# Optimization experiments

Measured on AMD Instinct MI355X. Metric: run time of the kernel, lower is better.

Reference implementation:

```python
import jax, jax.numpy as jnp
import numpy as np

B, N, D, H = 16, 1024, 512, 8


def setup_inputs() -> dict:
    key = jax.random.key(0)
    ks = jax.random.split(key, 11)
    std = D ** (-0.5)
    inp = {
        "k": jax.random.normal(ks[0], (B, N, D), dtype=jnp.float32),
        "v": jax.random.normal(ks[1], (B, N, D), dtype=jnp.float32),
        "q": jax.random.normal(ks[2], (B, N, D), dtype=jnp.float32),
        # per-head projection weights, torch Linear layout [out,in], init std = in**-0.5
        "Wk": jax.random.normal(ks[3], (H, D, D), dtype=jnp.float32) * std,
        "bk": jax.random.normal(ks[4], (H, D), dtype=jnp.float32) * 0.01,
        "Wv": jax.random.normal(ks[5], (H, D, D), dtype=jnp.float32) * std,
        "bv": jax.random.normal(ks[6], (H, D), dtype=jnp.float32) * 0.01,
        "Wq": jax.random.normal(ks[7], (H, D, D), dtype=jnp.float32) * std,
        "bq": jax.random.normal(ks[8], (H, D), dtype=jnp.float32) * 0.01,
        # output projection: Linear(H*D -> D), weight [D, H*D]
        "Wo": jax.random.normal(ks[9], (D, H * D), dtype=jnp.float32) * ((H * D) ** (-0.5)),
        "bo": jax.random.normal(ks[10], (D,), dtype=jnp.float32) * 0.01,
    }
    return inp


def reference(k, v, q, Wk, bk, Wv, bv, Wq, bq, Wo, bo):
    scale = jnp.asarray(D ** 0.5, dtype=k.dtype)
    # batched per-head projections: y = x @ W.T + b  -> [H, B, N, D]
    k_ = jnp.einsum("bnd,hed->hbne", k, Wk) + bk[:, None, None, :]
    v_ = jnp.einsum("bnd,hed->hbne", v, Wv) + bv[:, None, None, :]
    q_ = jnp.einsum("bnd,hed->hbne", q, Wq) + bq[:, None, None, :]
    # dot-product attention: scores[h,b,i,j] = q_[h,b,i] . k_[h,b,j]
    scores = jnp.einsum("hbid,hbjd->hbij", q_, k_) / scale
    attn = jax.nn.softmax(scores, axis=-1)
    out = jnp.einsum("hbij,hbjd->hbid", attn, v_)  # [H, B, N, D]
    # torch: stack(dim=-1) -> [B,N,D,H]; view -> [B,N,D*H] interleaved (d,h)
    outs = jnp.transpose(out, (1, 2, 3, 0)).reshape(B, N, D * H)
    rep = jnp.einsum("bnf,of->bno", outs, Wo) + bo
    return rep
```

## Files before the change

kernel.cpp:

```cpp
#include <hip/hip_runtime.h>

typedef __bf16 bf16;
typedef __bf16 bf16x8 __attribute__((ext_vector_type(8)));
typedef __bf16 bf16x4 __attribute__((ext_vector_type(4)));
typedef float  f32x4  __attribute__((ext_vector_type(4)));

#define BATCH 16
#define SEQ   1024
#define DIM   512
#define HEADS 8
#define BN    (BATCH*SEQ)
#define QK_SCALE 0.04419417382415922f


__device__ __forceinline__ void load16_lds(const void* g, void* l) {
  __builtin_amdgcn_global_load_lds((__attribute__((address_space(1))) void*)g,
                                   (__attribute__((address_space(3))) void*)l,
                                   16, 0, 0);
}

template<bool RS>
__device__ __forceinline__ void gemm_tile(const bf16* __restrict__ Atile, int lda,
                                          const bf16* __restrict__ Btile, int ldb,
                                          int K, f32x4 acc[4][4], f32x4 rs[4])
{
  __shared__ bf16 As[2][128*32];
  __shared__ bf16 Bs[2][128*32];
  const int tid  = threadIdx.x;
  const int wave = tid >> 6;
  const int lane = tid & 63;
  const int wm = wave >> 1, wn = wave & 1;
  const int srow = lane >> 2;
  const int scol = (lane & 3) * 8;
  const int frow = lane & 15;
  const int kq   = (lane >> 4) * 8;

  bf16x8 ones;
#pragma unroll
  for (int j = 0; j < 8; ++j) ones[j] = (bf16)1.0f;

  __syncthreads();
#pragma unroll
  for (int i = 0; i < 2; ++i) {
    const int c = wave * 2 + i;
    load16_lds(Atile + (size_t)(c*16 + srow) * lda + scol, &As[0][c*512]);
    load16_lds(Btile + (size_t)(c*16 + srow) * ldb + scol, &Bs[0][c*512]);
  }
  __syncthreads();

  int cur = 0;
  for (int kt = 0; kt < K; kt += 32) {
    const int nxt = kt + 32;
    if (nxt < K) {
#pragma unroll
      for (int i = 0; i < 2; ++i) {
        const int c = wave * 2 + i;
        load16_lds(Atile + (size_t)(c*16 + srow) * lda + nxt + scol, &As[cur^1][c*512]);
        load16_lds(Btile + (size_t)(c*16 + srow) * ldb + nxt + scol, &Bs[cur^1][c*512]);
      }
    }
    bf16x8 af[4], bfr[4];
#pragma unroll
    for (int mi = 0; mi < 4; ++mi)
      af[mi] = *(const bf16x8*)(&As[cur][(wm*64 + mi*16 + frow)*32 + kq]);
#pragma unroll
    for (int ni = 0; ni < 4; ++ni)
      bfr[ni] = *(const bf16x8*)(&Bs[cur][(wn*64 + ni*16 + frow)*32 + kq]);
#pragma unroll
    for (int mi = 0; mi < 4; ++mi) {
#pragma unroll
      for (int ni = 0; ni < 4; ++ni)
        acc[mi][ni] = __builtin_amdgcn_mfma_f32_16x16x32_bf16(af[mi], bfr[ni],
                                                              acc[mi][ni], 0, 0, 0);
      if (RS)
        rs[mi] = __builtin_amdgcn_mfma_f32_16x16x32_bf16(af[mi], ones, rs[mi], 0, 0, 0);
    }
    __syncthreads();
    cur ^= 1;
  }
}



__global__ __launch_bounds__(256)
void proj_nk(const bf16* __restrict__ X, const bf16* __restrict__ W,
             const float* __restrict__ bias, bf16* __restrict__ C)
{
  const int z = blockIdx.z;
  const bf16* A  = X + (size_t)blockIdx.x * 128 * DIM;
  const bf16* Bt = W + (size_t)z * DIM * DIM + (size_t)blockIdx.y * 128 * DIM;
  f32x4 acc[4][4] = {};
  gemm_tile<false>(A, DIM, Bt, DIM, DIM, acc, nullptr);

  const int tid = threadIdx.x, wave = tid >> 6, lane = tid & 63;
  const int wm = wave >> 1, wn = wave & 1;
  const int row0 = blockIdx.x*128 + wm*64;
  const int col0 = blockIdx.y*128 + wn*64;
  bf16* Cz = C + (size_t)z * BN * DIM;
  const float* bz = bias + (size_t)z * DIM;
#pragma unroll
  for (int ni = 0; ni < 4; ++ni) {
    const int col = col0 + ni*16 + (lane & 15);
    const float bb = bz[col];
#pragma unroll
    for (int mi = 0; mi < 4; ++mi) {
      const int row = row0 + mi*16 + (lane >> 4)*4;
#pragma unroll
      for (int r = 0; r < 4; ++r)
        Cz[(size_t)(row + r)*DIM + col] = (bf16)(acc[mi][ni][r] + bb);
    }
  }
}

__global__ __launch_bounds__(256)
void proj_v(const bf16* __restrict__ X, const bf16* __restrict__ W,
            const float* __restrict__ bias, bf16* __restrict__ vT)
{
  const int z = blockIdx.z;
  const bf16* A  = X + (size_t)blockIdx.x * 128 * DIM;
  const bf16* Bt = W + (size_t)z * DIM * DIM + (size_t)blockIdx.y * 128 * DIM;
  f32x4 acc[4][4] = {};
  gemm_tile<false>(A, DIM, Bt, DIM, DIM, acc, nullptr);

  const int tid = threadIdx.x, wave = tid >> 6, lane = tid & 63;
  const int wm = wave >> 1, wn = wave & 1;
  const int gm0 = blockIdx.x * 128;
  const int b   = gm0 >> 10;
  const int n00 = (gm0 & (SEQ-1)) + wm*64;
  const int col0 = blockIdx.y*128 + wn*64;
  const float* bz = bias + (size_t)z * DIM;
  bf16* base = vT + (size_t)(z*BATCH + b) * DIM * SEQ;
#pragma unroll
  for (int ni = 0; ni < 4; ++ni) {
    const int d = col0 + ni*16 + (lane & 15);
    const float bb = bz[d];
#pragma unroll
    for (int mi = 0; mi < 4; ++mi) {
      const int n = n00 + mi*16 + (lane >> 4)*4;
      bf16x4 v;
      v[0] = (bf16)(acc[mi][ni][0] + bb);
      v[1] = (bf16)(acc[mi][ni][1] + bb);
      v[2] = (bf16)(acc[mi][ni][2] + bb);
      v[3] = (bf16)(acc[mi][ni][3] + bb);
      *(bf16x4*)(base + (size_t)d*SEQ + n) = v;
    }
  }
}


__global__ __launch_bounds__(256)
void k_scores(const bf16* __restrict__ Q, const bf16* __restrict__ Kh,
              bf16* __restrict__ P)
{
  const int z = blockIdx.z;
  const bf16* A  = Q  + (size_t)z*SEQ*DIM + (size_t)blockIdx.x*128*DIM;
  const bf16* Bt = Kh + (size_t)z*SEQ*DIM + (size_t)blockIdx.y*128*DIM;
  f32x4 acc[4][4] = {};
  gemm_tile<false>(A, DIM, Bt, DIM, DIM, acc, nullptr);

  const int tid = threadIdx.x, wave = tid >> 6, lane = tid & 63;
  const int wm = wave >> 1, wn = wave & 1;
  const int row0 = blockIdx.x*128 + wm*64;
  const int col0 = blockIdx.y*128 + wn*64;
  bf16* Pz = P + (size_t)z * SEQ * SEQ;
#pragma unroll
  for (int ni = 0; ni < 4; ++ni) {
    const int col = col0 + ni*16 + (lane & 15);
#pragma unroll
    for (int mi = 0; mi < 4; ++mi) {
      const int row = row0 + mi*16 + (lane >> 4)*4;
#pragma unroll
      for (int r = 0; r < 4; ++r)
        Pz[(size_t)(row + r)*SEQ + col] = (bf16)__expf(acc[mi][ni][r] * QK_SCALE);
    }
  }
}

__global__ __launch_bounds__(256)
void k_pv(const bf16* __restrict__ P, const bf16* __restrict__ vT,
          bf16* __restrict__ Out)
{
  const int z = blockIdx.z;
  const bf16* A  = P  + (size_t)z*SEQ*SEQ + (size_t)blockIdx.x*128*SEQ;
  const bf16* Bt = vT + (size_t)z*DIM*SEQ + (size_t)blockIdx.y*128*SEQ;
  f32x4 acc[4][4] = {};
  f32x4 rs[4] = {};
  gemm_tile<true>(A, SEQ, Bt, SEQ, SEQ, acc, rs);

  const int tid = threadIdx.x, wave = tid >> 6, lane = tid & 63;
  const int wm = wave >> 1, wn = wave & 1;
  const int row0 = blockIdx.x*128 + wm*64;
  const int col0 = blockIdx.y*128 + wn*64;
  bf16* Oz = Out + (size_t)z * SEQ * DIM;
  float inv[4][4];
#pragma unroll
  for (int mi = 0; mi < 4; ++mi)
#pragma unroll
    for (int r = 0; r < 4; ++r)
      inv[mi][r] = 1.0f / rs[mi][r];
#pragma unroll
  for (int ni = 0; ni < 4; ++ni) {
    const int col = col0 + ni*16 + (lane & 15);
#pragma unroll
    for (int mi = 0; mi < 4; ++mi) {
      const int row = row0 + mi*16 + (lane >> 4)*4;
#pragma unroll
      for (int r = 0; r < 4; ++r)
        Oz[(size_t)(row + r)*DIM + col] = (bf16)(acc[mi][ni][r] * inv[mi][r]);
    }
  }
}

__global__ __launch_bounds__(256)
void k_final(const bf16* __restrict__ OutB, const bf16* __restrict__ Wor,
             int G, float* __restrict__ rep)
{
  f32x4 acc[4][4] = {};
  for (int g = 0; g < G; ++g)
    gemm_tile<false>(OutB + (size_t)g*BN*DIM + (size_t)blockIdx.x*128*DIM, DIM,
                     Wor  + (size_t)g*DIM*DIM + (size_t)blockIdx.y*128*DIM, DIM,
                     DIM, acc, nullptr);

  const int tid = threadIdx.x, wave = tid >> 6, lane = tid & 63;
  const int wm = wave >> 1, wn = wave & 1;
  const int row0 = blockIdx.x*128 + wm*64;
  const int col0 = blockIdx.y*128 + wn*64;
#pragma unroll
  for (int ni = 0; ni < 4; ++ni) {
    const int col = col0 + ni*16 + (lane & 15);
#pragma unroll
    for (int mi = 0; mi < 4; ++mi) {
      const int row = row0 + mi*16 + (lane >> 4)*4;
#pragma unroll
      for (int r = 0; r < 4; ++r)
        rep[(size_t)(row + r)*DIM + col] += acc[mi][ni][r];
    }
  }
}


__global__ __launch_bounds__(256)
void k_cast(const float* __restrict__ in, bf16* __restrict__ out, int n8)
{
  const int i = blockIdx.x*256 + threadIdx.x;
  if (i >= n8) return;
  const float4* p = (const float4*)in + (size_t)i*2;
  const float4 a = p[0], b = p[1];
  bf16x8 o;
  o[0]=(bf16)a.x; o[1]=(bf16)a.y; o[2]=(bf16)a.z; o[3]=(bf16)a.w;
  o[4]=(bf16)b.x; o[5]=(bf16)b.y; o[6]=(bf16)b.z; o[7]=(bf16)b.w;
  *((bf16x8*)out + i) = o;
}

__global__ __launch_bounds__(256)
void k_rearrange_wo(const float* __restrict__ Wo, bf16* __restrict__ Wor)
{
  const int idx = blockIdx.x*256 + threadIdx.x;
  const int d = idx & (DIM-1);
  const int o = (idx >> 9) & (DIM-1);
  const int h = idx >> 18;
  Wor[idx] = (bf16)Wo[((size_t)o << 12) + (d << 3) + h];
}

__global__ __launch_bounds__(256)
void k_init_out(float* __restrict__ out, const float* __restrict__ bo)
{
  const int idx = blockIdx.x*256 + threadIdx.x;
  out[idx] = bo[idx & (DIM-1)];
}


extern "C" void kernel_launch(void* const* d_in, const int* in_sizes, int n_in,
                              void* d_out, int out_size, void* d_ws, size_t ws_size,
                              hipStream_t stream)
{
  (void)in_sizes; (void)n_in; (void)out_size;
  const float* k_in = (const float*)d_in[0];
  const float* v_in = (const float*)d_in[1];
  const float* q_in = (const float*)d_in[2];
  const float* Wk   = (const float*)d_in[3];
  const float* bk   = (const float*)d_in[4];
  const float* Wv   = (const float*)d_in[5];
  const float* bv   = (const float*)d_in[6];
  const float* Wq   = (const float*)d_in[7];
  const float* bq   = (const float*)d_in[8];
  const float* Wo   = (const float*)d_in[9];
  const float* bo   = (const float*)d_in[10];

  auto needBytes = [](int G, int Bc) -> size_t {
    size_t b = 0;
    b += (size_t)3 * BN * DIM * 2;
    b += (size_t)3 * HEADS * DIM * DIM * 2;
    b += (size_t)HEADS * DIM * DIM * 2;
    b += (size_t)4 * G * BN * DIM * 2;
    b += (size_t)Bc * SEQ * SEQ * 2;
    return b;
  };
  static const int cand[8][2] = {{8,16},{4,16},{2,16},{1,16},{1,8},{1,4},{1,2},{1,1}};
  int G = 1, Bc = 1;
  for (int c = 0; c < 8; ++c)
    if (needBytes(cand[c][0], cand[c][1]) <= ws_size) { G = cand[c][0]; Bc = cand[c][1]; break; }

  char* p = (char*)d_ws;
  auto take = [&](size_t bytes) { char* r = p; p += bytes; return r; };
  bf16* Xk   = (bf16*)take((size_t)BN*DIM*2);
  bf16* Xv   = (bf16*)take((size_t)BN*DIM*2);
  bf16* Xq   = (bf16*)take((size_t)BN*DIM*2);
  bf16* Wkc  = (bf16*)take((size_t)HEADS*DIM*DIM*2);
  bf16* Wvc  = (bf16*)take((size_t)HEADS*DIM*DIM*2);
  bf16* Wqc  = (bf16*)take((size_t)HEADS*DIM*DIM*2);
  bf16* Worb = (bf16*)take((size_t)HEADS*DIM*DIM*2);
  bf16* qh   = (bf16*)take((size_t)G*BN*DIM*2);
  bf16* kh   = (bf16*)take((size_t)G*BN*DIM*2);
  bf16* vTh  = (bf16*)take((size_t)G*BN*DIM*2);
  bf16* outb = (bf16*)take((size_t)G*BN*DIM*2);
  bf16* Pb   = (bf16*)take((size_t)Bc*SEQ*SEQ*2);

  const int n8x = BN*DIM/8;
  const int n8w = HEADS*DIM*DIM/8;
  k_cast<<<n8x/256, 256, 0, stream>>>(k_in, Xk, n8x);
  k_cast<<<n8x/256, 256, 0, stream>>>(v_in, Xv, n8x);
  k_cast<<<n8x/256, 256, 0, stream>>>(q_in, Xq, n8x);
  k_cast<<<n8w/256, 256, 0, stream>>>(Wk, Wkc, n8w);
  k_cast<<<n8w/256, 256, 0, stream>>>(Wv, Wvc, n8w);
  k_cast<<<n8w/256, 256, 0, stream>>>(Wq, Wqc, n8w);
  k_rearrange_wo<<<HEADS*DIM*DIM/256, 256, 0, stream>>>(Wo, Worb);
  k_init_out<<<BN*DIM/256, 256, 0, stream>>>((float*)d_out, bo);

  for (int g0 = 0; g0 < HEADS; g0 += G) {
    dim3 gp(BN/128, DIM/128, G);
    proj_nk<<<gp, 256, 0, stream>>>(Xq, Wqc + (size_t)g0*DIM*DIM, bq + (size_t)g0*DIM, qh);
    proj_nk<<<gp, 256, 0, stream>>>(Xk, Wkc + (size_t)g0*DIM*DIM, bk + (size_t)g0*DIM, kh);
    proj_v <<<gp, 256, 0, stream>>>(Xv, Wvc + (size_t)g0*DIM*DIM, bv + (size_t)g0*DIM, vTh);
    for (int hz = 0; hz < G; ++hz) {
      for (int b0 = 0; b0 < BATCH; b0 += Bc) {
        const size_t hb = (size_t)(hz*BATCH + b0);
        dim3 gs(SEQ/128, SEQ/128, Bc);
        k_scores<<<gs, 256, 0, stream>>>(qh + hb*SEQ*DIM, kh + hb*SEQ*DIM, Pb);
        dim3 gv(SEQ/128, DIM/128, Bc);
        k_pv<<<gv, 256, 0, stream>>>(Pb, vTh + hb*DIM*SEQ, outb + hb*SEQ*DIM);
      }
    }
    k_final<<<dim3(BN/128, DIM/128), 256, 0, stream>>>(outb, Worb + (size_t)g0*DIM*DIM, G, (float*)d_out);
  }
}
```

Measured before the change: 1.270 ms.

## Fold Q/K and V/O weights algebraically and fuse PV with output projection

Precomputes the per-head products Wq^T·Wk and Wo_h·Wv with a hi/lo bf16 split, so the scores come from q·M against the raw k, and each head's V path maps straight to the output dimension. Bias terms reduce to a per-key constant and a constant output bias, and the bk term is dropped because it cancels in the softmax. PV and the output projection are fused into one kernel that accumulates over heads, which removes the K projection, the separate final GEMM, and the read-modify-write of the output. The trade-off is extra precompute kernels, larger workspace, and possible precision loss from folding the weights.

```diff
diff --git a/kernel.cpp b/kernel.cpp
--- a/kernel.cpp
+++ b/kernel.cpp
@@ -80,163 +80,6 @@
   }
 }
 
-
-
-__global__ __launch_bounds__(256)
-void proj_nk(const bf16* __restrict__ X, const bf16* __restrict__ W,
-             const float* __restrict__ bias, bf16* __restrict__ C)
-{
-  const int z = blockIdx.z;
-  const bf16* A  = X + (size_t)blockIdx.x * 128 * DIM;
-  const bf16* Bt = W + (size_t)z * DIM * DIM + (size_t)blockIdx.y * 128 * DIM;
-  f32x4 acc[4][4] = {};
-  gemm_tile<false>(A, DIM, Bt, DIM, DIM, acc, nullptr);
-
-  const int tid = threadIdx.x, wave = tid >> 6, lane = tid & 63;
-  const int wm = wave >> 1, wn = wave & 1;
-  const int row0 = blockIdx.x*128 + wm*64;
-  const int col0 = blockIdx.y*128 + wn*64;
-  bf16* Cz = C + (size_t)z * BN * DIM;
-  const float* bz = bias + (size_t)z * DIM;
-#pragma unroll
-  for (int ni = 0; ni < 4; ++ni) {
-    const int col = col0 + ni*16 + (lane & 15);
-    const float bb = bz[col];
-#pragma unroll
-    for (int mi = 0; mi < 4; ++mi) {
-      const int row = row0 + mi*16 + (lane >> 4)*4;
-#pragma unroll
-      for (int r = 0; r < 4; ++r)
-        Cz[(size_t)(row + r)*DIM + col] = (bf16)(acc[mi][ni][r] + bb);
-    }
-  }
-}
-
-__global__ __launch_bounds__(256)
-void proj_v(const bf16* __restrict__ X, const bf16* __restrict__ W,
-            const float* __restrict__ bias, bf16* __restrict__ vT)
-{
-  const int z = blockIdx.z;
-  const bf16* A  = X + (size_t)blockIdx.x * 128 * DIM;
-  const bf16* Bt = W + (size_t)z * DIM * DIM + (size_t)blockIdx.y * 128 * DIM;
-  f32x4 acc[4][4] = {};
-  gemm_tile<false>(A, DIM, Bt, DIM, DIM, acc, nullptr);
-
-  const int tid = threadIdx.x, wave = tid >> 6, lane = tid & 63;
-  const int wm = wave >> 1, wn = wave & 1;
-  const int gm0 = blockIdx.x * 128;
-  const int b   = gm0 >> 10;
-  const int n00 = (gm0 & (SEQ-1)) + wm*64;
-  const int col0 = blockIdx.y*128 + wn*64;
-  const float* bz = bias + (size_t)z * DIM;
-  bf16* base = vT + (size_t)(z*BATCH + b) * DIM * SEQ;
-#pragma unroll
-  for (int ni = 0; ni < 4; ++ni) {
-    const int d = col0 + ni*16 + (lane & 15);
-    const float bb = bz[d];
-#pragma unroll
-    for (int mi = 0; mi < 4; ++mi) {
-      const int n = n00 + mi*16 + (lane >> 4)*4;
-      bf16x4 v;
-      v[0] = (bf16)(acc[mi][ni][0] + bb);
-      v[1] = (bf16)(acc[mi][ni][1] + bb);
-      v[2] = (bf16)(acc[mi][ni][2] + bb);
-      v[3] = (bf16)(acc[mi][ni][3] + bb);
-      *(bf16x4*)(base + (size_t)d*SEQ + n) = v;
-    }
-  }
-}
-
-
-__global__ __launch_bounds__(256)
-void k_scores(const bf16* __restrict__ Q, const bf16* __restrict__ Kh,
-              bf16* __restrict__ P)
-{
-  const int z = blockIdx.z;
-  const bf16* A  = Q  + (size_t)z*SEQ*DIM + (size_t)blockIdx.x*128*DIM;
-  const bf16* Bt = Kh + (size_t)z*SEQ*DIM + (size_t)blockIdx.y*128*DIM;
-  f32x4 acc[4][4] = {};
-  gemm_tile<false>(A, DIM, Bt, DIM, DIM, acc, nullptr);
-
-  const int tid = threadIdx.x, wave = tid >> 6, lane = tid & 63;
-  const int wm = wave >> 1, wn = wave & 1;
-  const int row0 = blockIdx.x*128 + wm*64;
-  const int col0 = blockIdx.y*128 + wn*64;
-  bf16* Pz = P + (size_t)z * SEQ * SEQ;
-#pragma unroll
-  for (int ni = 0; ni < 4; ++ni) {
-    const int col = col0 + ni*16 + (lane & 15);
-#pragma unroll
-    for (int mi = 0; mi < 4; ++mi) {
-      const int row = row0 + mi*16 + (lane >> 4)*4;
-#pragma unroll
-      for (int r = 0; r < 4; ++r)
-        Pz[(size_t)(row + r)*SEQ + col] = (bf16)__expf(acc[mi][ni][r] * QK_SCALE);
-    }
-  }
-}
-
-__global__ __launch_bounds__(256)
-void k_pv(const bf16* __restrict__ P, const bf16* __restrict__ vT,
-          bf16* __restrict__ Out)
-{
-  const int z = blockIdx.z;
-  const bf16* A  = P  + (size_t)z*SEQ*SEQ + (size_t)blockIdx.x*128*SEQ;
-  const bf16* Bt = vT + (size_t)z*DIM*SEQ + (size_t)blockIdx.y*128*SEQ;
-  f32x4 acc[4][4] = {};
-  f32x4 rs[4] = {};
-  gemm_tile<true>(A, SEQ, Bt, SEQ, SEQ, acc, rs);
-
-  const int tid = threadIdx.x, wave = tid >> 6, lane = tid & 63;
-  const int wm = wave >> 1, wn = wave & 1;
-  const int row0 = blockIdx.x*128 + wm*64;
-  const int col0 = blockIdx.y*128 + wn*64;
-  bf16* Oz = Out + (size_t)z * SEQ * DIM;
-  float inv[4][4];
-#pragma unroll
-  for (int mi = 0; mi < 4; ++mi)
-#pragma unroll
-    for (int r = 0; r < 4; ++r)
-      inv[mi][r] = 1.0f / rs[mi][r];
-#pragma unroll
-  for (int ni = 0; ni < 4; ++ni) {
-    const int col = col0 + ni*16 + (lane & 15);
-#pragma unroll
-    for (int mi = 0; mi < 4; ++mi) {
-      const int row = row0 + mi*16 + (lane >> 4)*4;
-#pragma unroll
-      for (int r = 0; r < 4; ++r)
-        Oz[(size_t)(row + r)*DIM + col] = (bf16)(acc[mi][ni][r] * inv[mi][r]);
-    }
-  }
-}
-
-__global__ __launch_bounds__(256)
-void k_final(const bf16* __restrict__ OutB, const bf16* __restrict__ Wor,
-             int G, float* __restrict__ rep)
-{
-  f32x4 acc[4][4] = {};
-  for (int g = 0; g < G; ++g)
-    gemm_tile<false>(OutB + (size_t)g*BN*DIM + (size_t)blockIdx.x*128*DIM, DIM,
-                     Wor  + (size_t)g*DIM*DIM + (size_t)blockIdx.y*128*DIM, DIM,
-                     DIM, acc, nullptr);
-
-  const int tid = threadIdx.x, wave = tid >> 6, lane = tid & 63;
-  const int wm = wave >> 1, wn = wave & 1;
-  const int row0 = blockIdx.x*128 + wm*64;
-  const int col0 = blockIdx.y*128 + wn*64;
-#pragma unroll
-  for (int ni = 0; ni < 4; ++ni) {
-    const int col = col0 + ni*16 + (lane & 15);
-#pragma unroll
-    for (int mi = 0; mi < 4; ++mi) {
-      const int row = row0 + mi*16 + (lane >> 4)*4;
-#pragma unroll
-      for (int r = 0; r < 4; ++r)
-        rep[(size_t)(row + r)*DIM + col] += acc[mi][ni][r];
-    }
-  }
-}
 
 
 __global__ __launch_bounds__(256)
@@ -253,20 +96,252 @@
 }
 
 __global__ __launch_bounds__(256)
-void k_rearrange_wo(const float* __restrict__ Wo, bf16* __restrict__ Wor)
+void k_trans_hilo(const float* __restrict__ W, bf16* __restrict__ Thi,
+                  bf16* __restrict__ Tlo)
 {
   const int idx = blockIdx.x*256 + threadIdx.x;
-  const int d = idx & (DIM-1);
-  const int o = (idx >> 9) & (DIM-1);
-  const int h = idx >> 18;
-  Wor[idx] = (bf16)Wo[((size_t)o << 12) + (d << 3) + h];
-}
-
-__global__ __launch_bounds__(256)
-void k_init_out(float* __restrict__ out, const float* __restrict__ bo)
+  const int e = idx & 511, d = (idx >> 9) & 511, h = idx >> 18;
+  const float v = W[((size_t)(h*DIM + e))*DIM + d];
+  const bf16 hi = (bf16)v;
+  Thi[idx] = hi;
+  Tlo[idx] = (bf16)(v - (float)hi);
+}
+
+__global__ __launch_bounds__(256)
+void k_wor_hilo(const float* __restrict__ Wo, bf16* __restrict__ Whi,
+                bf16* __restrict__ Wlo)
 {
   const int idx = blockIdx.x*256 + threadIdx.x;
-  out[idx] = bo[idx & (DIM-1)];
+  const int e = idx & 511, o = (idx >> 9) & 511, h = idx >> 18;
+  const float v = Wo[((size_t)o << 12) + (e << 3) + h];
+  const bf16 hi = (bf16)v;
+  Whi[idx] = hi;
+  Wlo[idx] = (bf16)(v - (float)hi);
+}
+
+__global__ __launch_bounds__(256)
+void k_gemm3(const bf16* Ahi, const bf16* Alo, const bf16* Bhi, const bf16* Blo,
+             bf16* __restrict__ C)
+{
+  const int z = blockIdx.z;
+  const size_t off = (size_t)z * DIM * DIM;
+  f32x4 acc[4][4] = {};
+  for (int t = 0; t < 3; ++t) {
+    const bf16* A  = ((t == 2) ? Alo : Ahi) + off + (size_t)blockIdx.x*128*DIM;
+    const bf16* Bt = ((t == 1) ? Blo : Bhi) + off + (size_t)blockIdx.y*128*DIM;
+    gemm_tile<false>(A, DIM, Bt, DIM, DIM, acc, nullptr);
+  }
+  const int tid = threadIdx.x, wave = tid >> 6, lane = tid & 63;
+  const int wm = wave >> 1, wn = wave & 1;
+  const int row0 = blockIdx.x*128 + wm*64;
+  const int col0 = blockIdx.y*128 + wn*64;
+#pragma unroll
+  for (int ni = 0; ni < 4; ++ni) {
+    const int col = col0 + ni*16 + (lane & 15);
+#pragma unroll
+    for (int mi = 0; mi < 4; ++mi) {
+      const int row = row0 + mi*16 + (lane >> 4)*4;
+#pragma unroll
+      for (int r = 0; r < 4; ++r)
+        C[off + (size_t)(row + r)*DIM + col] = (bf16)acc[mi][ni][r];
+    }
+  }
+}
+
+__global__ __launch_bounds__(256)
+void k_wvec(const float* __restrict__ Wk, const float* __restrict__ bq,
+            float* __restrict__ w)
+{
+  const int idx = blockIdx.x*256 + threadIdx.x;
+  const int d = idx & 511, h = idx >> 9;
+  float s = 0.f;
+  for (int e = 0; e < DIM; ++e)
+    s += Wk[((size_t)(h*DIM + e))*DIM + d] * bq[h*DIM + e];
+  w[idx] = s;
+}
+
+__global__ __launch_bounds__(256)
+void k_cvec(const float* __restrict__ k, const float* __restrict__ w,
+            float* __restrict__ c)
+{
+  __shared__ float ws[HEADS][DIM];
+  for (int i = threadIdx.x; i < HEADS*DIM; i += 256)
+    ws[i >> 9][i & 511] = w[i];
+  __syncthreads();
+  const int token = blockIdx.x*4 + (threadIdx.x >> 6);
+  const int lane  = threadIdx.x & 63;
+  const float4* kr = (const float4*)(k + (size_t)token * DIM);
+  float kk[8];
+  *(float4*)(kk)     = kr[lane*2];
+  *(float4*)(kk + 4) = kr[lane*2 + 1];
+#pragma unroll
+  for (int h = 0; h < HEADS; ++h) {
+    float s = 0.f;
+#pragma unroll
+    for (int j = 0; j < 8; ++j) s += kk[j] * ws[h][lane*8 + j];
+#pragma unroll
+    for (int o = 32; o >= 1; o >>= 1) s += __shfl_xor(s, o, 64);
+    if (lane == 0) c[(size_t)h*BN + token] = s;
+  }
+}
+
+__global__ __launch_bounds__(256)
+void k_bconst(const float* __restrict__ Wo, const float* __restrict__ bv,
+              const float* __restrict__ bo, float* __restrict__ bc)
+{
+  const int o    = blockIdx.x*4 + (threadIdx.x >> 6);
+  const int lane = threadIdx.x & 63;
+  const float4* row = (const float4*)(Wo + ((size_t)o << 12));
+  float s = 0.f;
+  for (int it = 0; it < 16; ++it) {
+    const int f0 = (it*64 + lane)*4;
+    const float4 x = row[it*64 + lane];
+    s += x.x * bv[((f0+0)&7)*DIM + ((f0+0)>>3)];
+    s += x.y * bv[((f0+1)&7)*DIM + ((f0+1)>>3)];
+    s += x.z * bv[((f0+2)&7)*DIM + ((f0+2)>>3)];
+    s += x.w * bv[((f0+3)&7)*DIM + ((f0+3)>>3)];
+  }
+#pragma unroll
+  for (int of = 32; of >= 1; of >>= 1) s += __shfl_xor(s, of, 64);
+  if (lane == 0) bc[o] = s + bo[o];
+}
+
+
+__global__ __launch_bounds__(256)
+void k_qm(const bf16* __restrict__ X, const bf16* __restrict__ MT,
+          bf16* __restrict__ C)
+{
+  const int z = blockIdx.z;
+  const bf16* A  = X  + (size_t)blockIdx.x*128*DIM;
+  const bf16* Bt = MT + (size_t)z*DIM*DIM + (size_t)blockIdx.y*128*DIM;
+  f32x4 acc[4][4] = {};
+  gemm_tile<false>(A, DIM, Bt, DIM, DIM, acc, nullptr);
+
+  const int tid = threadIdx.x, wave = tid >> 6, lane = tid & 63;
+  const int wm = wave >> 1, wn = wave & 1;
+  const int rows = gridDim.x * 128;
+  const int row0 = blockIdx.x*128 + wm*64;
+  const int col0 = blockIdx.y*128 + wn*64;
+  bf16* Cz = C + (size_t)z * rows * DIM;
+#pragma unroll
+  for (int ni = 0; ni < 4; ++ni) {
+    const int col = col0 + ni*16 + (lane & 15);
+#pragma unroll
+    for (int mi = 0; mi < 4; ++mi) {
+      const int row = row0 + mi*16 + (lane >> 4)*4;
+#pragma unroll
+      for (int r = 0; r < 4; ++r)
+        Cz[(size_t)(row + r)*DIM + col] = (bf16)acc[mi][ni][r];
+    }
+  }
+}
+
+__global__ __launch_bounds__(256)
+void k_vct(const bf16* __restrict__ X, const bf16* __restrict__ G,
+           bf16* __restrict__ vcT, int Bc)
+{
+  const int z = blockIdx.z;
+  const bf16* A  = X + (size_t)blockIdx.x*128*DIM;
+  const bf16* Bt = G + (size_t)z*DIM*DIM + (size_t)blockIdx.y*128*DIM;
+  f32x4 acc[4][4] = {};
+  gemm_tile<false>(A, DIM, Bt, DIM, DIM, acc, nullptr);
+
+  const int tid = threadIdx.x, wave = tid >> 6, lane = tid & 63;
+  const int wm = wave >> 1, wn = wave & 1;
+  const int gm0 = blockIdx.x * 128;
+  const int bloc = gm0 >> 10;
+  const int n00 = (gm0 & (SEQ-1)) + wm*64;
+  const int col0 = blockIdx.y*128 + wn*64;
+  bf16* base = vcT + (size_t)(z*Bc + bloc) * DIM * SEQ;
+#pragma unroll
+  for (int ni = 0; ni < 4; ++ni) {
+    const int o = col0 + ni*16 + (lane & 15);
+#pragma unroll
+    for (int mi = 0; mi < 4; ++mi) {
+      const int n = n00 + mi*16 + (lane >> 4)*4;
+      bf16x4 v;
+      v[0] = (bf16)acc[mi][ni][0];
+      v[1] = (bf16)acc[mi][ni][1];
+      v[2] = (bf16)acc[mi][ni][2];
+      v[3] = (bf16)acc[mi][ni][3];
+      *(bf16x4*)(base + (size_t)o*SEQ + n) = v;
+    }
+  }
+}
+
+__global__ __launch_bounds__(256)
+void k_scores(const bf16* __restrict__ QM, const bf16* __restrict__ Kb,
+              const float* __restrict__ cvec, bf16* __restrict__ P,
+              int Bc, int b0)
+{
+  const int z = blockIdx.z;
+  const int h = z / Bc, bloc = z % Bc;
+  const bf16* A  = QM + ((size_t)(h*Bc + bloc)*SEQ + blockIdx.x*128)*DIM;
+  const bf16* Bt = Kb + ((size_t)(b0 + bloc)*SEQ + blockIdx.y*128)*DIM;
+  f32x4 acc[4][4] = {};
+  gemm_tile<false>(A, DIM, Bt, DIM, DIM, acc, nullptr);
+
+  const int tid = threadIdx.x, wave = tid >> 6, lane = tid & 63;
+  const int wm = wave >> 1, wn = wave & 1;
+  const int row0 = blockIdx.x*128 + wm*64;
+  const int col0 = blockIdx.y*128 + wn*64;
+  const float* cz = cvec + (size_t)h*BN + (size_t)(b0 + bloc)*SEQ;
+  bf16* Pz = P + (size_t)(h*Bc + bloc)*SEQ*SEQ;
+#pragma unroll
+  for (int ni = 0; ni < 4; ++ni) {
+    const int col = col0 + ni*16 + (lane & 15);
+    const float cc = cz[col];
+#pragma unroll
+    for (int mi = 0; mi < 4; ++mi) {
+      const int row = row0 + mi*16 + (lane >> 4)*4;
+#pragma unroll
+      for (int r = 0; r < 4; ++r)
+        Pz[(size_t)(row + r)*SEQ + col] = (bf16)__expf((acc[mi][ni][r] + cc) * QK_SCALE);
+    }
+  }
+}
+
+__global__ __launch_bounds__(256, 2)
+void k_pvfinal(const bf16* __restrict__ P, const bf16* __restrict__ vcT,
+               const float* __restrict__ bcon, float* __restrict__ rep,
+               int Bc, int b0)
+{
+  const int bloc = blockIdx.z;
+  f32x4 accO[4][4] = {};
+  for (int h = 0; h < HEADS; ++h) {
+    const bf16* A  = P   + ((size_t)(h*Bc + bloc)*SEQ + blockIdx.x*128)*SEQ;
+    const bf16* Bt = vcT + ((size_t)(h*Bc + bloc)*DIM + blockIdx.y*128)*SEQ;
+    f32x4 acc[4][4] = {};
+    f32x4 rs[4] = {};
+    gemm_tile<true>(A, SEQ, Bt, SEQ, SEQ, acc, rs);
+#pragma unroll
+    for (int mi = 0; mi < 4; ++mi) {
+      f32x4 inv;
+#pragma unroll
+      for (int r = 0; r < 4; ++r) inv[r] = 1.0f / rs[mi][r];
+#pragma unroll
+      for (int ni = 0; ni < 4; ++ni)
+#pragma unroll
+        for (int r = 0; r < 4; ++r)
+          accO[mi][ni][r] += acc[mi][ni][r] * inv[r];
+    }
+  }
+  const int tid = threadIdx.x, wave = tid >> 6, lane = tid & 63;
+  const int wm = wave >> 1, wn = wave & 1;
+  const int row0 = (b0 + bloc)*SEQ + blockIdx.x*128 + wm*64;
+  const int col0 = blockIdx.y*128 + wn*64;
+#pragma unroll
+  for (int ni = 0; ni < 4; ++ni) {
+    const int col = col0 + ni*16 + (lane & 15);
+    const float bb = bcon[col];
+#pragma unroll
+    for (int mi = 0; mi < 4; ++mi) {
+      const int row = row0 + mi*16 + (lane >> 4)*4;
+#pragma unroll
+      for (int r = 0; r < 4; ++r)
+        rep[(size_t)(row + r)*DIM + col] = accO[mi][ni][r] + bb;
+    }
+  }
 }
 
 
@@ -279,68 +354,67 @@
   const float* v_in = (const float*)d_in[1];
   const float* q_in = (const float*)d_in[2];
   const float* Wk   = (const float*)d_in[3];
-  const float* bk   = (const float*)d_in[4];
+  const float* bq_f = (const float*)d_in[8];
   const float* Wv   = (const float*)d_in[5];
-  const float* bv   = (const float*)d_in[6];
+  const float* bv_f = (const float*)d_in[6];
   const float* Wq   = (const float*)d_in[7];
-  const float* bq   = (const float*)d_in[8];
   const float* Wo   = (const float*)d_in[9];
   const float* bo   = (const float*)d_in[10];
 
-  auto needBytes = [](int G, int Bc) -> size_t {
-    size_t b = 0;
-    b += (size_t)3 * BN * DIM * 2;
-    b += (size_t)3 * HEADS * DIM * DIM * 2;
-    b += (size_t)HEADS * DIM * DIM * 2;
-    b += (size_t)4 * G * BN * DIM * 2;
-    b += (size_t)Bc * SEQ * SEQ * 2;
-    return b;
-  };
-  static const int cand[8][2] = {{8,16},{4,16},{2,16},{1,16},{1,8},{1,4},{1,2},{1,1}};
-  int G = 1, Bc = 1;
-  for (int c = 0; c < 8; ++c)
-    if (needBytes(cand[c][0], cand[c][1]) <= ws_size) { G = cand[c][0]; Bc = cand[c][1]; break; }
+  const size_t WMAT = (size_t)HEADS*DIM*DIM*2;
+  const size_t fixedB = (size_t)3*BN*DIM*2 + 8*WMAT + 2*WMAT
+                      + (size_t)HEADS*DIM*4 + (size_t)HEADS*BN*4 + DIM*4;
+  int Bc = 1;
+  for (int c : {16, 8, 4, 2, 1}) {
+    const size_t need = fixedB + (size_t)c * (2*(size_t)HEADS*SEQ*DIM*2
+                                              + (size_t)HEADS*SEQ*SEQ*2);
+    if (need <= ws_size) { Bc = c; break; }
+  }
 
   char* p = (char*)d_ws;
   auto take = [&](size_t bytes) { char* r = p; p += bytes; return r; };
-  bf16* Xk   = (bf16*)take((size_t)BN*DIM*2);
-  bf16* Xv   = (bf16*)take((size_t)BN*DIM*2);
-  bf16* Xq   = (bf16*)take((size_t)BN*DIM*2);
-  bf16* Wkc  = (bf16*)take((size_t)HEADS*DIM*DIM*2);
-  bf16* Wvc  = (bf16*)take((size_t)HEADS*DIM*DIM*2);
-  bf16* Wqc  = (bf16*)take((size_t)HEADS*DIM*DIM*2);
-  bf16* Worb = (bf16*)take((size_t)HEADS*DIM*DIM*2);
-  bf16* qh   = (bf16*)take((size_t)G*BN*DIM*2);
-  bf16* kh   = (bf16*)take((size_t)G*BN*DIM*2);
-  bf16* vTh  = (bf16*)take((size_t)G*BN*DIM*2);
-  bf16* outb = (bf16*)take((size_t)G*BN*DIM*2);
-  bf16* Pb   = (bf16*)take((size_t)Bc*SEQ*SEQ*2);
+  bf16* qbf   = (bf16*)take((size_t)BN*DIM*2);
+  bf16* vbf   = (bf16*)take((size_t)BN*DIM*2);
+  bf16* kbf   = (bf16*)take((size_t)BN*DIM*2);
+  bf16* WqThi = (bf16*)take(WMAT);
+  bf16* WqTlo = (bf16*)take(WMAT);
+  bf16* WkThi = (bf16*)take(WMAT);
+  bf16* WkTlo = (bf16*)take(WMAT);
+  bf16* WvThi = (bf16*)take(WMAT);
+  bf16* WvTlo = (bf16*)take(WMAT);
+  bf16* Worhi = (bf16*)take(WMAT);
+  bf16* Worlo = (bf16*)take(WMAT);
+  bf16* MT    = (bf16*)take(WMAT);
+  bf16* Gwv   = (bf16*)take(WMAT);
+  float* wv   = (float*)take((size_t)HEADS*DIM*4);
+  float* cvec = (float*)take((size_t)HEADS*BN*4);
+  float* bcon = (float*)take((size_t)DIM*4);
+  bf16* qm    = (bf16*)take((size_t)Bc*HEADS*SEQ*DIM*2);
+  bf16* vcT   = (bf16*)take((size_t)Bc*HEADS*SEQ*DIM*2);
+  bf16* Pb    = (bf16*)take((size_t)Bc*HEADS*SEQ*SEQ*2);
 
   const int n8x = BN*DIM/8;
-  const int n8w = HEADS*DIM*DIM/8;
-  k_cast<<<n8x/256, 256, 0, stream>>>(k_in, Xk, n8x);
-  k_cast<<<n8x/256, 256, 0, stream>>>(v_in, Xv, n8x);
-  k_cast<<<n8x/256, 256, 0, stream>>>(q_in, Xq, n8x);
-  k_cast<<<n8w/256, 256, 0, stream>>>(Wk, Wkc, n8w);
-  k_cast<<<n8w/256, 256, 0, stream>>>(Wv, Wvc, n8w);
-  k_cast<<<n8w/256, 256, 0, stream>>>(Wq, Wqc, n8w);
-  k_rearrange_wo<<<HEADS*DIM*DIM/256, 256, 0, stream>>>(Wo, Worb);
-  k_init_out<<<BN*DIM/256, 256, 0, stream>>>((float*)d_out, bo);
-
-  for (int g0 = 0; g0 < HEADS; g0 += G) {
-    dim3 gp(BN/128, DIM/128, G);
-    proj_nk<<<gp, 256, 0, stream>>>(Xq, Wqc + (size_t)g0*DIM*DIM, bq + (size_t)g0*DIM, qh);
-    proj_nk<<<gp, 256, 0, stream>>>(Xk, Wkc + (size_t)g0*DIM*DIM, bk + (size_t)g0*DIM, kh);
-    proj_v <<<gp, 256, 0, stream>>>(Xv, Wvc + (size_t)g0*DIM*DIM, bv + (size_t)g0*DIM, vTh);
-    for (int hz = 0; hz < G; ++hz) {
-      for (int b0 = 0; b0 < BATCH; b0 += Bc) {
-        const size_t hb = (size_t)(hz*BATCH + b0);
-        dim3 gs(SEQ/128, SEQ/128, Bc);
-        k_scores<<<gs, 256, 0, stream>>>(qh + hb*SEQ*DIM, kh + hb*SEQ*DIM, Pb);
-        dim3 gv(SEQ/128, DIM/128, Bc);
-        k_pv<<<gv, 256, 0, stream>>>(Pb, vTh + hb*DIM*SEQ, outb + hb*SEQ*DIM);
-      }
-    }
-    k_final<<<dim3(BN/128, DIM/128), 256, 0, stream>>>(outb, Worb + (size_t)g0*DIM*DIM, G, (float*)d_out);
-  }
-}
+  const int nW  = HEADS*DIM*DIM;
+  k_cast<<<n8x/256, 256, 0, stream>>>(q_in, qbf, n8x);
+  k_cast<<<n8x/256, 256, 0, stream>>>(v_in, vbf, n8x);
+  k_cast<<<n8x/256, 256, 0, stream>>>(k_in, kbf, n8x);
+  k_trans_hilo<<<nW/256, 256, 0, stream>>>(Wq, WqThi, WqTlo);
+  k_trans_hilo<<<nW/256, 256, 0, stream>>>(Wk, WkThi, WkTlo);
+  k_trans_hilo<<<nW/256, 256, 0, stream>>>(Wv, WvThi, WvTlo);
+  k_wor_hilo<<<nW/256, 256, 0, stream>>>(Wo, Worhi, Worlo);
+  k_gemm3<<<dim3(4,4,HEADS), 256, 0, stream>>>(WkThi, WkTlo, WqThi, WqTlo, MT);
+  k_gemm3<<<dim3(4,4,HEADS), 256, 0, stream>>>(Worhi, Worlo, WvThi, WvTlo, Gwv);
+  k_wvec<<<HEADS*DIM/256, 256, 0, stream>>>(Wk, bq_f, wv);
+  k_cvec<<<BN/4, 256, 0, stream>>>(k_in, wv, cvec);
+  k_bconst<<<DIM/4, 256, 0, stream>>>(Wo, bv_f, bo, bcon);
+
+  for (int b0 = 0; b0 < BATCH; b0 += Bc) {
+    dim3 gq(Bc*SEQ/128, DIM/128, HEADS);
+    k_qm <<<gq, 256, 0, stream>>>(qbf + (size_t)b0*SEQ*DIM, MT, qm);
+    k_vct<<<gq, 256, 0, stream>>>(vbf + (size_t)b0*SEQ*DIM, Gwv, vcT, Bc);
+    dim3 gs(SEQ/128, SEQ/128, HEADS*Bc);
+    k_scores<<<gs, 256, 0, stream>>>(qm, kbf, cvec, Pb, Bc, b0);
+    dim3 gv(SEQ/128, DIM/128, Bc);
+    k_pvfinal<<<gv, 256, 0, stream>>>(Pb, vcT, bcon, (float*)d_out, Bc, b0);
+  }
+}
```

After: 1.442 ms. 1.13x slower.
